# Performance work log

Measured on AMD Instinct MI355X. Metric: run time of the kernel, lower is better.

Reference implementation:

```python
import jax, jax.numpy as jnp
import numpy as np

HEAD_DIM = 256
N_HEADS = 8
ROPE_BASE = 10000.0
EPS = 1e-6


def _rms(x):
    xf = x.astype(jnp.float32)
    return xf * jax.lax.rsqrt(jnp.mean(xf * xf, axis=-1, keepdims=True) + EPS)


def _rotate_half(x):
    x1, x2 = jnp.split(x, 2, axis=-1)
    return jnp.concatenate([-x2, x1], axis=-1)


def _mlp(h, wg, wu, wd):
    # Gemma gated MLP with gelu_pytorch_tanh activation
    return (jax.nn.gelu(h @ wg, approximate=True) * (h @ wu)) @ wd


def _qkv(h, wq, wk, wv):
    B, S, _ = h.shape
    q = (h @ wq).reshape(B, S, N_HEADS, HEAD_DIM).transpose(0, 2, 1, 3)  # [B,H,S,Dh]
    k = (h @ wk).reshape(B, S, HEAD_DIM)                                  # MQA: 1 kv head
    v = (h @ wv).reshape(B, S, HEAD_DIM)
    return q, k, v


def _forward(x_prefix, x_expert, attention_mask, adarms_cond, position_ids,
             p_ln1, p_wq, p_wk, p_wv, p_wo, p_ln2, p_wgate, p_wup, p_wdown,
             e_ada1_w, e_ada1_b, e_wq, e_wk, e_wv, e_wo, e_ada2_w, e_ada2_b,
             e_wgate, e_wup, e_wdown):
    B, S1, Dp = x_prefix.shape
    S2 = x_expert.shape[1]

    # --- pre-attention norms: plain Gemma RMSNorm (prefix), AdaRMS (expert) ---
    h_p = _rms(x_prefix) * (1.0 + p_ln1)
    mod1 = adarms_cond @ e_ada1_w + e_ada1_b                  # [B, 3*De]
    sc1, sh1, g1 = jnp.split(mod1, 3, axis=-1)
    h_e = _rms(x_expert) * (1.0 + sc1[:, None]) + sh1[:, None]
    gate1_e = g1[:, None]                                      # [B,1,De]

    # --- concatenated QKV across the two streams ---
    q_p, k_p, v_p = _qkv(h_p, p_wq, p_wk, p_wv)
    q_e, k_e, v_e = _qkv(h_e, e_wq, e_wk, e_wv)
    q = jnp.concatenate([q_p, q_e], axis=2)                    # [B,H,S,Dh]
    k = jnp.concatenate([k_p, k_e], axis=1)                    # [B,S,Dh]
    v = jnp.concatenate([v_p, v_e], axis=1)

    # --- rotary embedding on joint positions ---
    inv_freq = 1.0 / (ROPE_BASE ** (jnp.arange(0, HEAD_DIM, 2, dtype=jnp.float32) / HEAD_DIM))
    ang = position_ids.astype(jnp.float32)[..., None] * inv_freq
    emb = jnp.concatenate([ang, ang], axis=-1)                 # [B,S,Dh]
    cos, sin = jnp.cos(emb), jnp.sin(emb)
    q = q * cos[:, None] + _rotate_half(q) * sin[:, None]
    k = k * cos + _rotate_half(k) * sin

    # --- eager MQA attention ---
    scaling = HEAD_DIM ** -0.5
    scores = jnp.einsum('bhqd,bkd->bhqk', q, k) * scaling + attention_mask
    probs = jax.nn.softmax(scores.astype(jnp.float32), axis=-1)
    att = jnp.einsum('bhqk,bkd->bhqd', probs, v)
    att = att.transpose(0, 2, 1, 3).reshape(B, S1 + S2, N_HEADS * HEAD_DIM)

    # --- prefix stream: o_proj, residual, RMSNorm, gated MLP, residual ---
    res_p = x_prefix + att[:, :S1] @ p_wo
    h2_p = _rms(res_p) * (1.0 + p_ln2)
    out_p = res_p + _mlp(h2_p, p_wgate, p_wup, p_wdown)

    # --- expert stream: gated residuals from AdaRMS ---
    res_e = x_expert + gate1_e * (att[:, S1:] @ e_wo)
    mod2 = adarms_cond @ e_ada2_w + e_ada2_b
    sc2, sh2, g2 = jnp.split(mod2, 3, axis=-1)
    h2_e = _rms(res_e) * (1.0 + sc2[:, None]) + sh2[:, None]
    out_e = res_e + g2[:, None] * _mlp(h2_e, e_wgate, e_wup, e_wdown)
    return out_p, out_e


def setup_inputs() -> dict:
    key = jax.random.key(0)
    ks = iter(jax.random.split(key, 32))
    B, S1, S2 = 4, 768, 64
    Dp, De, Dh, H = 2048, 1024, 256, 8
    Fp, Fe = 16384, 4096

    def w(shape, s=0.02):
        return jax.random.normal(next(ks), shape, dtype=jnp.float32) * s

    return dict(
        x_prefix=jax.random.normal(next(ks), (B, S1, Dp), dtype=jnp.float32),
        x_expert=jax.random.normal(next(ks), (B, S2, De), dtype=jnp.float32),
        attention_mask=jnp.zeros((B, 1, S1 + S2, S1 + S2), dtype=jnp.float32),
        adarms_cond=jax.random.normal(next(ks), (B, De), dtype=jnp.float32),
        position_ids=jnp.sort(jax.random.randint(next(ks), (B, S1 + S2), 0, S1 + S2), axis=-1),
        p_ln1=jnp.zeros((Dp,), jnp.float32),
        p_wq=w((Dp, H * Dh)), p_wk=w((Dp, Dh)), p_wv=w((Dp, Dh)), p_wo=w((H * Dh, Dp)),
        p_ln2=jnp.zeros((Dp,), jnp.float32),
        p_wgate=w((Dp, Fp)), p_wup=w((Dp, Fp)), p_wdown=w((Fp, Dp)),
        e_ada1_w=w((De, 3 * De)), e_ada1_b=jnp.zeros((3 * De,), jnp.float32),
        e_wq=w((De, H * Dh)), e_wk=w((De, Dh)), e_wv=w((De, Dh)), e_wo=w((H * Dh, De)),
        e_ada2_w=w((De, 3 * De)), e_ada2_b=jnp.zeros((3 * De,), jnp.float32),
        e_wgate=w((De, Fe)), e_wup=w((De, Fe)), e_wdown=w((Fe, De)),
    )


def reference(x_prefix, x_expert, attention_mask, adarms_cond, position_ids,
              p_ln1, p_wq, p_wk, p_wv, p_wo, p_ln2, p_wgate, p_wup, p_wdown,
              e_ada1_w, e_ada1_b, e_wq, e_wk, e_wv, e_wo, e_ada2_w, e_ada2_b,
              e_wgate, e_wup, e_wdown):
    return _forward(x_prefix, x_expert, attention_mask, adarms_cond, position_ids,
                    p_ln1, p_wq, p_wk, p_wv, p_wo, p_ln2, p_wgate, p_wup, p_wdown,
                    e_ada1_w, e_ada1_b, e_wq, e_wk, e_wv, e_wo, e_ada2_w, e_ada2_b,
                    e_wgate, e_wup, e_wdown)
```

## Files before the change

kernel.cpp:

```cpp
#include <hip/hip_runtime.h>
#include <stdint.h>

typedef unsigned short ushort_t;
typedef __attribute__((ext_vector_type(8))) short short8;
typedef __attribute__((ext_vector_type(4))) float f32x4;

#define DEVINL __device__ __forceinline__

DEVINL ushort_t f2bf(float f){
  union { float f; uint32_t u; } v; v.f = f;
  uint32_t u = v.u;
  uint32_t r = (u + 0x7fffu + ((u >> 16) & 1u)) >> 16;
  return (ushort_t)r;
}
DEVINL float bf2f(ushort_t h){
  union { uint32_t u; float f; } v; v.u = ((uint32_t)h) << 16;
  return v.f;
}
DEVINL f32x4 mfma16(short8 a, short8 b, f32x4 c){
  return __builtin_amdgcn_mfma_f32_16x16x32_bf16(a, b, c, 0, 0, 0);
}
DEVINL void gload_lds16(const void* g, void* l){
  __builtin_amdgcn_global_load_lds((const __attribute__((address_space(1))) void*)g,
                                   (__attribute__((address_space(3))) void*)l, 16, 0, 0);
}
DEVINL float gelu_tanh(float x){
  return 0.5f * x * (1.f + tanhf(0.7978845608028654f * (x + 0.044715f * x * x * x)));
}

#define BAR() __builtin_amdgcn_s_barrier()
#define LGK0() asm volatile("s_waitcnt lgkmcnt(0)" ::: "memory")
#define VMC4() asm volatile("s_waitcnt vmcnt(4)" ::: "memory")
#define VMC0() asm volatile("s_waitcnt vmcnt(0)" ::: "memory")
#define PRIO1() __builtin_amdgcn_s_setprio(1)
#define PRIO0() __builtin_amdgcn_s_setprio(0)

__global__ void transpose_bf16(const float* __restrict__ W, ushort_t* __restrict__ Wt,
                               int K, int N)
{
  __shared__ ushort_t tile[64 * 65];
  const int t = threadIdx.x;
  const int k0 = blockIdx.y * 64, n0 = blockIdx.x * 64;
#pragma unroll
  for (int rr = 0; rr < 4; ++rr){
    const int row = rr * 16 + (t >> 4);
    const int c4 = (t & 15) * 4;
    float4 v = *(const float4*)&W[(size_t)(k0 + row) * N + n0 + c4];
    ushort_t* dst = &tile[row * 65 + c4];
    dst[0] = f2bf(v.x); dst[1] = f2bf(v.y); dst[2] = f2bf(v.z); dst[3] = f2bf(v.w);
  }
  __syncthreads();
  const int n = t >> 2, kc = (t & 3) * 16;
  __align__(16) ushort_t tmp[16];
#pragma unroll
  for (int j = 0; j < 16; ++j) tmp[j] = tile[(kc + j) * 65 + n];
  ushort_t* out = &Wt[(size_t)(n0 + n) * K + k0 + kc];
  *(short8*)&out[0] = *(short8*)&tmp[0];
  *(short8*)&out[8] = *(short8*)&tmp[8];
}

__global__ void mod_kernel(const float* __restrict__ cond,
                           const float* __restrict__ w1, const float* __restrict__ b1,
                           const float* __restrict__ w2, const float* __restrict__ b2,
                           float* __restrict__ mod1, float* __restrict__ mod2)
{
  __shared__ float cs[1024];
  const int bid = blockIdx.x, tid = threadIdx.x;
  const int which = bid / 48, rem = bid % 48, b = rem / 12, j0 = (rem % 12) * 256;
  const float* W = which ? w2 : w1;
  const float* bias = which ? b2 : b1;
  float* out = which ? mod2 : mod1;
#pragma unroll
  for (int i = 0; i < 4; ++i) cs[i * 256 + tid] = cond[b * 1024 + i * 256 + tid];
  __syncthreads();
  const int j = j0 + tid;
  float acc = bias[j];
  for (int k = 0; k < 1024; ++k) acc = fmaf(cs[k], W[(size_t)k * 3072 + j], acc);
  out[b * 3072 + j] = acc;
}

__global__ void rms_kernel(const float* __restrict__ x, ushort_t* __restrict__ out, int D,
                           const float* __restrict__ sw, const float* __restrict__ sh,
                           int mod_rpb, int mod_stride)
{
  const int row = blockIdx.x, tid = threadIdx.x;
  const float* xr = x + (size_t)row * D;
  const int nc = D >> 10;
  float ss = 0.f;
  for (int c = 0; c < nc; ++c){
    float4 v = *(const float4*)&xr[c * 1024 + tid * 4];
    ss += v.x * v.x + v.y * v.y + v.z * v.z + v.w * v.w;
  }
  for (int o = 32; o > 0; o >>= 1) ss += __shfl_xor(ss, o);
  __shared__ float red[4];
  if ((tid & 63) == 0) red[tid >> 6] = ss;
  __syncthreads();
  const float scale = rsqrtf((red[0] + red[1] + red[2] + red[3]) / (float)D + 1e-6f);
  const float* swp = sw;
  const float* shp = sh;
  if (mod_rpb){
    int bb = row / mod_rpb;
    swp += (size_t)bb * mod_stride;
    if (shp) shp += (size_t)bb * mod_stride;
  }
  for (int c = 0; c < nc; ++c){
    const int d = c * 1024 + tid * 4;
    float4 v = *(const float4*)&xr[d];
    float vv[4] = {v.x, v.y, v.z, v.w};
#pragma unroll
    for (int i = 0; i < 4; ++i){
      float tv = vv[i] * scale * (1.f + swp[d + i]);
      if (shp) tv += shp[d + i];
      out[(size_t)row * D + d + i] = f2bf(tv);
    }
  }
}

__global__ void rope_kernel(const ushort_t* __restrict__ qkv_p, const ushort_t* __restrict__ qkv_e,
                            const int* __restrict__ pos_ids,
                            ushort_t* __restrict__ q_all, ushort_t* __restrict__ k_all,
                            ushort_t* __restrict__ vT)
{
  const int tok = blockIdx.x, tid = threadIdx.x;
  int b, s;
  const ushort_t* src;
  if (tok < 3072){ b = tok / 768; s = tok - b * 768; src = qkv_p + (size_t)tok * 2560; }
  else { int te = tok - 3072; b = te >> 6; s = 768 + (te & 63); src = qkv_e + (size_t)te * 2560; }
  const int pos = pos_ids[b * 832 + s];
  __shared__ float cs[128], sn[128];
  if (tid < 128){
    float f = powf(10000.f, -(float)tid * (1.f / 128.f));
    float a = (float)pos * f;
    cs[tid] = cosf(a); sn[tid] = sinf(a);
  }
  __syncthreads();
#pragma unroll
  for (int c = 0; c < 10; ++c){
    const int n = c * 256 + tid;
    const float v = bf2f(src[n]);
    if (n < 2048){
      const int h = n >> 8, d = n & 255;
      const float o = bf2f(src[(h << 8) + ((d < 128) ? (d + 128) : (d - 128))]);
      const int dd = d & 127;
      const float r = (d < 128) ? v * cs[dd] - o * sn[dd] : v * cs[dd] + o * sn[dd];
      q_all[(((size_t)(b * 8 + h)) * 832 + s) * 256 + d] = f2bf(r);
    } else if (n < 2304){
      const int d = n - 2048;
      const float o = bf2f(src[2048 + ((d < 128) ? (d + 128) : (d - 128))]);
      const int dd = d & 127;
      const float r = (d < 128) ? v * cs[dd] - o * sn[dd] : v * cs[dd] + o * sn[dd];
      const int ck = d >> 3, e = d & 7;
      const int ck2 = ck ^ (s & 7);
      k_all[((size_t)(b * 832) + s) * 256 + (ck2 << 3) + e] = f2bf(r);
    } else {
      const int d = n - 2304;
      const int stile = s >> 6, sl = s & 63;
      const int cv = sl >> 3, e = sl & 7;
      const int cv2 = cv ^ (d & 7);
      vT[((size_t)(b * 256) + d) * 832 + (stile << 6) + (cv2 << 3) + e] = src[n];
    }
  }
}

__global__ void __launch_bounds__(256, 2)
attn_kernel(const ushort_t* __restrict__ q_all, const ushort_t* __restrict__ k_all,
            const ushort_t* __restrict__ vT, const float* __restrict__ mask,
            ushort_t* __restrict__ att)
{
  __shared__ __align__(16) ushort_t Ks[64 * 256];
  __shared__ __align__(16) ushort_t Vs[256 * 64];
  __shared__ __align__(16) ushort_t Ps[4][16 * 72];
  const int tid = threadIdx.x, lane = tid & 63, wid = tid >> 6;
  const int l15 = lane & 15, lg = lane >> 4;
  const int qt = blockIdx.x, h = blockIdx.y, b = blockIdx.z;
  const int q0 = qt * 64 + wid * 16;
  const int x7 = l15 & 7;

  short8 qf[8];
  {
    const ushort_t* qr = q_all + (((size_t)(b * 8 + h) * 832) + q0 + l15) * 256;
#pragma unroll
    for (int s = 0; s < 8; ++s) qf[s] = *(const short8*)&qr[s * 32 + lg * 8];
  }

  f32x4 accO[16] = {};
  float mrow[4] = {-3.0e38f, -3.0e38f, -3.0e38f, -3.0e38f};
  float lrow[4] = {0.f, 0.f, 0.f, 0.f};

  for (int kt = 0; kt < 13; ++kt){
    const int s0 = kt * 64;
#pragma unroll
    for (int i = 0; i < 8; ++i){
      const int o = i * 256 + tid;
      gload_lds16(k_all + ((size_t)(b * 832) + s0 + (o >> 5)) * 256 + (o & 31) * 8, &Ks[o * 8]);
      gload_lds16(vT + ((size_t)(b * 256) + (o >> 3)) * 832 + s0 + (o & 7) * 8, &Vs[o * 8]);
    }
    __syncthreads();

    f32x4 sc[4] = {};
#pragma unroll
    for (int s = 0; s < 8; ++s){
#pragma unroll
      for (int nf = 0; nf < 4; ++nf){
        short8 kb = *(const short8*)&Ks[(nf * 16 + l15) * 256 + (((s * 4 + lg) ^ x7) << 3)];
        sc[nf] = mfma16(qf[s], kb, sc[nf]);
      }
    }
#pragma unroll
    for (int nf = 0; nf < 4; ++nf){
#pragma unroll
      for (int r = 0; r < 4; ++r){
        const int q = q0 + lg * 4 + r;
        const int kk = s0 + nf * 16 + l15;
        sc[nf][r] = sc[nf][r] * 0.0625f + mask[((size_t)b * 832 + q) * 832 + kk];
      }
    }
    float al[4];
#pragma unroll
    for (int r = 0; r < 4; ++r){
      float tm = fmaxf(fmaxf(sc[0][r], sc[1][r]), fmaxf(sc[2][r], sc[3][r]));
      tm = fmaxf(tm, __shfl_xor(tm, 1));
      tm = fmaxf(tm, __shfl_xor(tm, 2));
      tm = fmaxf(tm, __shfl_xor(tm, 4));
      tm = fmaxf(tm, __shfl_xor(tm, 8));
      const float mnew = fmaxf(mrow[r], tm);
      al[r] = __expf(mrow[r] - mnew);
      mrow[r] = mnew;
      float rs = 0.f;
#pragma unroll
      for (int nf = 0; nf < 4; ++nf){
        const float p = __expf(sc[nf][r] - mnew);
        rs += p;
        Ps[wid][(lg * 4 + r) * 72 + nf * 16 + l15] = f2bf(p);
      }
      rs += __shfl_xor(rs, 1);
      rs += __shfl_xor(rs, 2);
      rs += __shfl_xor(rs, 4);
      rs += __shfl_xor(rs, 8);
      lrow[r] = lrow[r] * al[r] + rs;
    }
#pragma unroll
    for (int nd = 0; nd < 16; ++nd){
#pragma unroll
      for (int r = 0; r < 4; ++r) accO[nd][r] *= al[r];
    }
#pragma unroll
    for (int ks = 0; ks < 2; ++ks){
      short8 pa = *(const short8*)&Ps[wid][l15 * 72 + ks * 32 + lg * 8];
#pragma unroll
      for (int nd = 0; nd < 16; ++nd){
        short8 vb = *(const short8*)&Vs[(nd * 16 + l15) * 64 + (((ks * 4 + lg) ^ x7) << 3)];
        accO[nd] = mfma16(pa, vb, accO[nd]);
      }
    }
    __syncthreads();
  }
#pragma unroll
  for (int nd = 0; nd < 16; ++nd){
#pragma unroll
    for (int r = 0; r < 4; ++r){
      const int q = q0 + lg * 4 + r;
      const int d = nd * 16 + l15;
      att[((size_t)(b * 832) + q) * 2048 + h * 256 + d] = f2bf(accO[nd][r] / lrow[r]);
    }
  }
}

template<int EPI>
__global__ void __launch_bounds__(256, 2)
gemm_bt(const ushort_t* __restrict__ A, int lda, int a_rpb, int a_bstride, int a_r0,
        const ushort_t* __restrict__ Bt, int ldb,
        void* __restrict__ Cv, int N, int K,
        const void* __restrict__ Xv,
        const float* __restrict__ gatep, int gate_stride, int gate_rpb,
        size_t pstride)
{
  __shared__ __align__(16) ushort_t As[128 * 64];
  __shared__ __align__(16) ushort_t Bs[128 * 64];
  const int tid = threadIdx.x;
  const int lane = tid & 63;
  const int l15 = lane & 15, lg = lane >> 4;
  const int wid = tid >> 6;
  const int wm = (wid >> 1) * 64, wn = (wid & 1) * 64;
  const int gx = gridDim.x, gy = gridDim.y, nwg = gx * gy;
  const int orig = blockIdx.y * gx + blockIdx.x;
  const int q = nwg >> 3, r = nwg & 7;
  const int xcd = orig & 7, lo = orig >> 3;
  const int wg = (xcd < r ? xcd * (q + 1) : r * (q + 1) + (xcd - r) * q) + lo;
  const int m0 = (wg % gy) * 128, n0 = (wg / gy) * 128;
  const int z = blockIdx.z;
  const int kbeg = z * K, kend = z * K + K;

  size_t abase[4], bbase[4];
  const int k8 = (tid & 7) * 8;
#pragma unroll
  for (int i = 0; i < 4; ++i){
    const int row = (i * 256 + tid) >> 3;
    const int rr = m0 + row;
    const int bb = rr / a_rpb;
    const int arow = bb * a_bstride + a_r0 + (rr - bb * a_rpb);
    abase[i] = (size_t)arow * lda + k8;
    bbase[i] = (size_t)(n0 + row) * ldb + k8;
  }

  f32x4 acc[4][4] = {};

  for (int kt = kbeg; kt < kend; kt += 64){
#pragma unroll
    for (int i = 0; i < 4; ++i){
      gload_lds16(A + abase[i] + kt, &As[(i * 256 + tid) * 8]);
      gload_lds16(Bt + bbase[i] + kt, &Bs[(i * 256 + tid) * 8]);
    }
    __syncthreads();
#pragma unroll
    for (int s = 0; s < 2; ++s){
      const int ko = s * 32 + lg * 8;
      short8 af[4], bfr[4];
#pragma unroll
      for (int i = 0; i < 4; ++i) af[i] = *(const short8*)&As[(wm + i * 16 + l15) * 64 + ko];
#pragma unroll
      for (int j = 0; j < 4; ++j) bfr[j] = *(const short8*)&Bs[(wn + j * 16 + l15) * 64 + ko];
#pragma unroll
      for (int i = 0; i < 4; ++i)
#pragma unroll
        for (int j = 0; j < 4; ++j)
          acc[i][j] = mfma16(af[i], bfr[j], acc[i][j]);
    }
    __syncthreads();
  }

#pragma unroll
  for (int i = 0; i < 4; ++i){
#pragma unroll
    for (int rr = 0; rr < 4; ++rr){
      const int m = m0 + wm + i * 16 + lg * 4 + rr;
#pragma unroll
      for (int j = 0; j < 4; ++j){
        const int n = n0 + wn + j * 16 + l15;
        const size_t idx = (size_t)m * N + n;
        const float v = acc[i][j][rr];
        if (EPI == 0){
          ((ushort_t*)Cv)[idx] = f2bf(v);
        } else if (EPI == 1){
          const float g = bf2f(((const ushort_t*)Xv)[idx]);
          ((ushort_t*)Cv)[idx] = f2bf(gelu_tanh(g) * v);
        } else if (EPI == 2){
          ((float*)Cv)[idx] = ((const float*)Xv)[idx] + v;
        } else if (EPI == 3){
          const int bb = m / gate_rpb;
          ((float*)Cv)[idx] = ((const float*)Xv)[idx] + gatep[(size_t)bb * gate_stride + n] * v;
        } else {
          ((float*)Cv)[(size_t)z * pstride + idx] = v;
        }
      }
    }
  }
}

#define MMAQ(AF, BF, MQ, NQ) \
  { _Pragma("unroll") for (int i_ = 0; i_ < 4; ++i_){ \
      _Pragma("unroll") for (int j_ = 0; j_ < 2; ++j_){ \
        _Pragma("unroll") for (int s_ = 0; s_ < 2; ++s_){ \
          acc[(MQ)*4 + i_][(NQ)*2 + j_] = \
            mfma16(AF[i_][s_], BF[j_][s_], acc[(MQ)*4 + i_][(NQ)*2 + j_]); } } } }

#define READA(F, BUF, OA) \
  { _Pragma("unroll") for (int i_ = 0; i_ < 4; ++i_){ \
      _Pragma("unroll") for (int s_ = 0; s_ < 2; ++s_){ \
        F[i_][s_] = *(const short8*)&(BUF)[OA[i_][s_]]; } } }

#define READB(F, BUF, OB) \
  { _Pragma("unroll") for (int j_ = 0; j_ < 2; ++j_){ \
      _Pragma("unroll") for (int s_ = 0; s_ < 2; ++s_){ \
        F[j_][s_] = *(const short8*)&(BUF)[OB[j_][s_]]; } } }

template<int EPI>
__global__ void __launch_bounds__(512, 1)
gemm8(const ushort_t* __restrict__ A, int lda,
      const ushort_t* __restrict__ Bt, int ldb,
      void* __restrict__ Cv, int N, int klen,
      const void* __restrict__ Xv, size_t pstride)
{
  __shared__ __align__(16) ushort_t As[2][256 * 64];
  __shared__ __align__(16) ushort_t Bs[2][256 * 64];

  const int tid = threadIdx.x;
  const int lane = tid & 63, wid = tid >> 6;
  const int l15 = lane & 15, lg = lane >> 4;
  const int wm = (wid >> 2) * 128, wn = (wid & 3) * 64;

  const int gx = gridDim.x, gy = gridDim.y, nwg = gx * gy;
  const int orig = blockIdx.y * gx + blockIdx.x;
  const int q = nwg >> 3, r = nwg & 7;
  const int xcd = orig & 7, lo = orig >> 3;
  const int wg = (xcd < r ? xcd * (q + 1) : r * (q + 1) + (xcd - r) * q) + lo;
  const int m0 = (wg % gy) * 256, n0 = (wg / gy) * 256;
  const int z = blockIdx.z;
  const size_t k0 = (size_t)z * klen;
  const int NT = klen >> 6;

  uint32_t offA0[4][2], offA1[4][2], offB0[2][2], offB1[2][2];
#pragma unroll
  for (int i = 0; i < 4; ++i){
#pragma unroll
    for (int s = 0; s < 2; ++s){
      int r0 = wm + 0 * 64 + i * 16 + l15;
      int r1 = wm + 1 * 64 + i * 16 + l15;
      offA0[i][s] = r0 * 64 + (((s * 4 + lg) ^ (r0 & 7)) << 3);
      offA1[i][s] = r1 * 64 + (((s * 4 + lg) ^ (r1 & 7)) << 3);
    }
  }
#pragma unroll
  for (int j = 0; j < 2; ++j){
#pragma unroll
    for (int s = 0; s < 2; ++s){
      int r0 = wn + 0 * 32 + j * 16 + l15;
      int r1 = wn + 1 * 32 + j * 16 + l15;
      offB0[j][s] = r0 * 64 + (((s * 4 + lg) ^ (r0 & 7)) << 3);
      offB1[j][s] = r1 * 64 + (((s * 4 + lg) ^ (r1 & 7)) << 3);
    }
  }

  const ushort_t* gptr[4][2];
  uint32_t ldso[2];
#pragma unroll
  for (int c = 0; c < 2; ++c){
    const int idx = c * 512 + tid;
    const int row = idx >> 3, slot = idx & 7;
    const uint32_t sw = (uint32_t)((slot ^ (row & 7)) << 3);
    ldso[c] = (uint32_t)idx * 8;
    gptr[0][c] = A  + (size_t)(m0 + row) * lda + k0 + sw;
    gptr[1][c] = A  + (size_t)(m0 + 128 + row) * lda + k0 + sw;
    gptr[2][c] = Bt + (size_t)(n0 + row) * ldb + k0 + sw;
    gptr[3][c] = Bt + (size_t)(n0 + 128 + row) * ldb + k0 + sw;
  }

  auto stage = [&](int buf, int half, int kt){
    ushort_t* base = (half < 2) ? &As[buf][(half & 1) * 8192] : &Bs[buf][(half & 1) * 8192];
#pragma unroll
    for (int c = 0; c < 2; ++c)
      gload_lds16(gptr[half][c] + kt, base + ldso[c]);
  };

  stage(0, 0, 0); stage(0, 1, 0); stage(0, 2, 0); stage(0, 3, 0);
  if (NT > 1){ stage(1, 2, 64); stage(1, 3, 64); VMC4(); } else { VMC0(); }
  BAR();

  short8 af[4][2], bq0[2][2], bq1[2][2];
  f32x4 acc[8][4] = {};

  for (int t = 0; t < NT; ++t){
    const int cur = t & 1, nxt = cur ^ 1;
    const int kc1 = (t + 1) << 6, kc2 = (t + 2) << 6;
    const ushort_t* Ac = As[cur];
    const ushort_t* Bc = Bs[cur];
    READA(af, Ac, offA0);
    READB(bq0, Bc, offB0);
    READB(bq1, Bc, offB1);
    if (t + 1 < NT){ stage(nxt, 0, kc1); stage(nxt, 1, kc1); }
    BAR(); LGK0();
    PRIO1(); MMAQ(af, bq0, 0, 0); MMAQ(af, bq1, 0, 1); PRIO0(); BAR();
    READA(af, Ac, offA1);
    if (t + 2 < NT){ stage(cur, 2, kc2); stage(cur, 3, kc2); VMC4(); } else { VMC0(); }
    BAR(); LGK0();
    PRIO1(); MMAQ(af, bq1, 1, 1); MMAQ(af, bq0, 1, 0); PRIO0(); BAR();
  }

#pragma unroll
  for (int i = 0; i < 8; ++i){
#pragma unroll
    for (int rr = 0; rr < 4; ++rr){
      const int m = m0 + wm + i * 16 + lg * 4 + rr;
#pragma unroll
      for (int j = 0; j < 4; ++j){
        const int n = n0 + wn + j * 16 + l15;
        const size_t idx = (size_t)m * N + n;
        const float v = acc[i][j][rr];
        if (EPI == 0){
          ((ushort_t*)Cv)[idx] = f2bf(v);
        } else if (EPI == 1){
          const float g = bf2f(((const ushort_t*)Xv)[idx]);
          ((ushort_t*)Cv)[idx] = f2bf(gelu_tanh(g) * v);
        } else {
          ((float*)Cv)[(size_t)z * pstride + idx] = v;
        }
      }
    }
  }
}

__global__ void reduce4(const float* __restrict__ part, const float* __restrict__ res,
                        float* __restrict__ out, int total4, size_t pstride)
{
  int i = blockIdx.x * blockDim.x + threadIdx.x;
  const int stride = gridDim.x * blockDim.x;
  for (; i < total4; i += stride){
    const size_t e = (size_t)i * 4;
    float4 a = *(const float4*)&res[e];
#pragma unroll
    for (int z = 0; z < 4; ++z){
      float4 p = *(const float4*)&part[(size_t)z * pstride + e];
      a.x += p.x; a.y += p.y; a.z += p.z; a.w += p.w;
    }
    *(float4*)&out[e] = a;
  }
}

__global__ void fuse_gelu(const float* __restrict__ pg, const float* __restrict__ pu,
                          ushort_t* __restrict__ out, int total4, size_t pstride)
{
  int i = blockIdx.x * blockDim.x + threadIdx.x;
  const int stride = gridDim.x * blockDim.x;
  for (; i < total4; i += stride){
    const size_t e = (size_t)i * 4;
    float4 g = *(const float4*)&pg[e];
    float4 u = *(const float4*)&pu[e];
#pragma unroll
    for (int z = 1; z < 4; ++z){
      float4 a = *(const float4*)&pg[(size_t)z * pstride + e];
      float4 b = *(const float4*)&pu[(size_t)z * pstride + e];
      g.x += a.x; g.y += a.y; g.z += a.z; g.w += a.w;
      u.x += b.x; u.y += b.y; u.z += b.z; u.w += b.w;
    }
    out[e + 0] = f2bf(gelu_tanh(g.x) * u.x);
    out[e + 1] = f2bf(gelu_tanh(g.y) * u.y);
    out[e + 2] = f2bf(gelu_tanh(g.z) * u.z);
    out[e + 3] = f2bf(gelu_tanh(g.w) * u.w);
  }
}

__global__ void reduce_gated(const float* __restrict__ part, size_t pstride, int nz,
                             const float* __restrict__ base, const float* __restrict__ gate,
                             int gstride, int rpb, int N,
                             float* __restrict__ out, int total4)
{
  int i = blockIdx.x * blockDim.x + threadIdx.x;
  const int stride = gridDim.x * blockDim.x;
  for (; i < total4; i += stride){
    const size_t e = (size_t)i * 4;
    const int row = (int)(e / N), n = (int)(e % N);
    const int b = row / rpb;
    float4 s = *(const float4*)&part[e];
    for (int z = 1; z < nz; ++z){
      float4 p = *(const float4*)&part[(size_t)z * pstride + e];
      s.x += p.x; s.y += p.y; s.z += p.z; s.w += p.w;
    }
    float4 bs = *(const float4*)&base[e];
    const float* gp = &gate[(size_t)b * gstride + n];
    bs.x += gp[0] * s.x; bs.y += gp[1] * s.y; bs.z += gp[2] * s.z; bs.w += gp[3] * s.w;
    *(float4*)&out[e] = bs;
  }
}

extern "C" void kernel_launch(void* const* d_in, const int* in_sizes, int n_in,
                              void* d_out, int out_size, void* d_ws, size_t ws_size,
                              hipStream_t stream)
{
  const float* x_prefix = (const float*)d_in[0];
  const float* x_expert = (const float*)d_in[1];
  const float* mask     = (const float*)d_in[2];
  const float* cond     = (const float*)d_in[3];
  const int*   pos      = (const int*)d_in[4];
  const float* p_ln1    = (const float*)d_in[5];
  const float* p_wq     = (const float*)d_in[6];
  const float* p_wk     = (const float*)d_in[7];
  const float* p_wv     = (const float*)d_in[8];
  const float* p_wo     = (const float*)d_in[9];
  const float* p_ln2    = (const float*)d_in[10];
  const float* p_wgate  = (const float*)d_in[11];
  const float* p_wup    = (const float*)d_in[12];
  const float* p_wdown  = (const float*)d_in[13];
  const float* e_ada1_w = (const float*)d_in[14];
  const float* e_ada1_b = (const float*)d_in[15];
  const float* e_wq     = (const float*)d_in[16];
  const float* e_wk     = (const float*)d_in[17];
  const float* e_wv     = (const float*)d_in[18];
  const float* e_wo     = (const float*)d_in[19];
  const float* e_ada2_w = (const float*)d_in[20];
  const float* e_ada2_b = (const float*)d_in[21];
  const float* e_wgate  = (const float*)d_in[22];
  const float* e_wup    = (const float*)d_in[23];
  const float* e_wdown  = (const float*)d_in[24];

  char* ws = (char*)d_ws;
  size_t off = 0;
  auto alloc = [&](size_t bytes) -> char* {
    char* p = ws + off;
    off += bytes;
    off = (off + 255) & ~(size_t)255;
    return p;
  };

  ushort_t* t_wqkv_p  = (ushort_t*)alloc((size_t)2560 * 2048 * 2);
  ushort_t* t_wo_p    = (ushort_t*)alloc((size_t)2048 * 2048 * 2);
  ushort_t* t_wgate_p = (ushort_t*)alloc((size_t)16384 * 2048 * 2);
  ushort_t* t_wup_p   = (ushort_t*)alloc((size_t)16384 * 2048 * 2);
  ushort_t* t_wdown_p = (ushort_t*)alloc((size_t)2048 * 16384 * 2);
  ushort_t* t_wqkv_e  = (ushort_t*)alloc((size_t)2560 * 1024 * 2);
  ushort_t* t_wo_e    = (ushort_t*)alloc((size_t)1024 * 2048 * 2);
  ushort_t* t_wgate_e = (ushort_t*)alloc((size_t)4096 * 1024 * 2);
  ushort_t* t_wup_e   = (ushort_t*)alloc((size_t)4096 * 1024 * 2);
  ushort_t* t_wdown_e = (ushort_t*)alloc((size_t)1024 * 4096 * 2);
  float* mod1 = (float*)alloc((size_t)4 * 3072 * 4);
  float* mod2 = (float*)alloc((size_t)4 * 3072 * 4);
  float* res_p = (float*)alloc((size_t)3072 * 2048 * 4);
  float* res_e = (float*)alloc((size_t)256 * 1024 * 4);
  ushort_t* h2_p = (ushort_t*)alloc((size_t)3072 * 2048 * 2);
  ushort_t* h2_e = (ushort_t*)alloc((size_t)256 * 1024 * 2);
  ushort_t* g_e  = (ushort_t*)alloc((size_t)256 * 4096 * 2);

  const size_t zone_off = off;
  ushort_t* h_p   = (ushort_t*)alloc((size_t)3072 * 2048 * 2);
  ushort_t* h_e   = (ushort_t*)alloc((size_t)256 * 1024 * 2);
  ushort_t* qkv_p = (ushort_t*)alloc((size_t)3072 * 2560 * 2);
  ushort_t* qkv_e = (ushort_t*)alloc((size_t)256 * 2560 * 2);
  ushort_t* q_all = (ushort_t*)alloc((size_t)4 * 8 * 832 * 256 * 2);
  ushort_t* k_all = (ushort_t*)alloc((size_t)4 * 832 * 256 * 2);
  ushort_t* vTb   = (ushort_t*)alloc((size_t)4 * 256 * 832 * 2);
  ushort_t* att   = (ushort_t*)alloc((size_t)4 * 832 * 2048 * 2);
  const size_t phase1_end = off;
  ushort_t* g_p = (ushort_t*)(ws + zone_off);

  float* partials = (float*)t_wgate_p;
  const size_t PSTRIDE_P = (size_t)3072 * 2048;
  float* pwo = (float*)(ws + zone_off);
  const size_t PSTRIDE_E = (size_t)256 * 1024;
  float* pg = (float*)t_wgate_p;
  float* pu = pg + (size_t)4 * 256 * 4096;
  float* pd = pu + (size_t)4 * 256 * 4096;
  const size_t PSTRIDE_GE = (size_t)256 * 4096;

  const size_t g_p_end = zone_off + (size_t)3072 * 16384 * 2;
  const size_t needed = (phase1_end > g_p_end) ? phase1_end : g_p_end;
  if (ws_size < needed) return;

  const int BIG = 1 << 30;

  transpose_bf16<<<dim3(2048/64, 2048/64), 256, 0, stream>>>(p_wq, t_wqkv_p, 2048, 2048);
  transpose_bf16<<<dim3(256/64, 2048/64), 256, 0, stream>>>(p_wk, t_wqkv_p + (size_t)2048*2048, 2048, 256);
  transpose_bf16<<<dim3(256/64, 2048/64), 256, 0, stream>>>(p_wv, t_wqkv_p + (size_t)2304*2048, 2048, 256);
  transpose_bf16<<<dim3(2048/64, 2048/64), 256, 0, stream>>>(p_wo, t_wo_p, 2048, 2048);
  transpose_bf16<<<dim3(16384/64, 2048/64), 256, 0, stream>>>(p_wgate, t_wgate_p, 2048, 16384);
  transpose_bf16<<<dim3(16384/64, 2048/64), 256, 0, stream>>>(p_wup, t_wup_p, 2048, 16384);
  transpose_bf16<<<dim3(2048/64, 16384/64), 256, 0, stream>>>(p_wdown, t_wdown_p, 16384, 2048);
  transpose_bf16<<<dim3(2048/64, 1024/64), 256, 0, stream>>>(e_wq, t_wqkv_e, 1024, 2048);
  transpose_bf16<<<dim3(256/64, 1024/64), 256, 0, stream>>>(e_wk, t_wqkv_e + (size_t)2048*1024, 1024, 256);
  transpose_bf16<<<dim3(256/64, 1024/64), 256, 0, stream>>>(e_wv, t_wqkv_e + (size_t)2304*1024, 1024, 256);
  transpose_bf16<<<dim3(1024/64, 2048/64), 256, 0, stream>>>(e_wo, t_wo_e, 2048, 1024);
  transpose_bf16<<<dim3(4096/64, 1024/64), 256, 0, stream>>>(e_wgate, t_wgate_e, 1024, 4096);
  transpose_bf16<<<dim3(4096/64, 1024/64), 256, 0, stream>>>(e_wup, t_wup_e, 1024, 4096);
  transpose_bf16<<<dim3(1024/64, 4096/64), 256, 0, stream>>>(e_wdown, t_wdown_e, 4096, 1024);

  mod_kernel<<<96, 256, 0, stream>>>(cond, e_ada1_w, e_ada1_b, e_ada2_w, e_ada2_b, mod1, mod2);

  rms_kernel<<<3072, 256, 0, stream>>>(x_prefix, h_p, 2048, p_ln1, nullptr, 0, 0);
  rms_kernel<<<256, 256, 0, stream>>>(x_expert, h_e, 1024, mod1, mod1 + 1024, 64, 3072);

  gemm_bt<0><<<dim3(20, 24), 256, 0, stream>>>(h_p, 2048, BIG, 0, 0, t_wqkv_p, 2048,
                                               qkv_p, 2560, 2048, nullptr, nullptr, 0, 1, 0);
  gemm_bt<0><<<dim3(20, 2), 256, 0, stream>>>(h_e, 1024, BIG, 0, 0, t_wqkv_e, 1024,
                                              qkv_e, 2560, 1024, nullptr, nullptr, 0, 1, 0);

  rope_kernel<<<3328, 256, 0, stream>>>(qkv_p, qkv_e, pos, q_all, k_all, vTb);

  attn_kernel<<<dim3(13, 8, 4), 256, 0, stream>>>(q_all, k_all, vTb, mask, att);

  gemm_bt<2><<<dim3(16, 24), 256, 0, stream>>>(att, 2048, 768, 832, 0, t_wo_p, 2048,
                                               res_p, 2048, 2048, x_prefix, nullptr, 0, 1, 0);
  gemm_bt<4><<<dim3(8, 2, 4), 256, 0, stream>>>(att, 2048, 64, 832, 768, t_wo_e, 2048,
                                                pwo, 1024, 512, nullptr, nullptr, 0, 1, PSTRIDE_E);
  reduce_gated<<<256, 256, 0, stream>>>(pwo, PSTRIDE_E, 4, x_expert, mod1 + 2048, 3072, 64, 1024,
                                        res_e, (256 * 1024) / 4);

  rms_kernel<<<3072, 256, 0, stream>>>(res_p, h2_p, 2048, p_ln2, nullptr, 0, 0);
  rms_kernel<<<256, 256, 0, stream>>>(res_e, h2_e, 1024, mod2, mod2 + 1024, 64, 3072);

  gemm8<0><<<dim3(64, 12, 1), 512, 0, stream>>>(h2_p, 2048, t_wgate_p, 2048,
                                                g_p, 16384, 2048, nullptr, 0);
  gemm8<1><<<dim3(64, 12, 1), 512, 0, stream>>>(h2_p, 2048, t_wup_p, 2048,
                                                g_p, 16384, 2048, g_p, 0);
  gemm8<4><<<dim3(8, 12, 4), 512, 0, stream>>>(g_p, 16384, t_wdown_p, 16384,
                                               partials, 2048, 4096, nullptr, PSTRIDE_P);
  reduce4<<<2048, 256, 0, stream>>>(partials, res_p, (float*)d_out,
                                    (3072 * 2048) / 4, PSTRIDE_P);

  gemm_bt<4><<<dim3(32, 2, 4), 256, 0, stream>>>(h2_e, 1024, BIG, 0, 0, t_wgate_e, 1024,
                                                 pg, 4096, 256, nullptr, nullptr, 0, 1, PSTRIDE_GE);
  gemm_bt<4><<<dim3(32, 2, 4), 256, 0, stream>>>(h2_e, 1024, BIG, 0, 0, t_wup_e, 1024,
                                                 pu, 4096, 256, nullptr, nullptr, 0, 1, PSTRIDE_GE);
  fuse_gelu<<<1024, 256, 0, stream>>>(pg, pu, g_e, (256 * 4096) / 4, PSTRIDE_GE);
  gemm_bt<4><<<dim3(8, 2, 8), 256, 0, stream>>>(g_e, 4096, BIG, 0, 0, t_wdown_e, 4096,
                                                pd, 1024, 512, nullptr, nullptr, 0, 1, PSTRIDE_E);
  reduce_gated<<<256, 256, 0, stream>>>(pd, PSTRIDE_E, 8, res_e, mod2 + 2048, 3072, 64, 1024,
                                        (float*)d_out + (size_t)3072 * 2048, (256 * 1024) / 4);
}
```

Before: 1.269 ms.

## Fuse prefix down-proj residual into GEMM, merge expert gate/up GEMMs

The prefix down projection moves from a split-K gemm8 with a separate reduce4 pass to a single gemm_bt<2> launch that adds the residual in its epilogue and writes straight to the output. The expert gate and up projections become one launch, which assumes t_wup_e sits right after t_wgate_e so the combined N is 8192. fuse_gelu now reads an interleaved gate/up partial buffer. This removes fp32 partial traffic and a launch, but swaps the tuned 512-thread gemm8 for gemm_bt on the largest GEMM with K=16384 and no split-K.

```diff
diff --git a/kernel.cpp b/kernel.cpp
--- a/kernel.cpp
+++ b/kernel.cpp
@@ -489,36 +489,22 @@
   }
 }
 
-__global__ void reduce4(const float* __restrict__ part, const float* __restrict__ res,
-                        float* __restrict__ out, int total4, size_t pstride)
+__global__ void fuse_gelu(const float* __restrict__ P, ushort_t* __restrict__ out,
+                          int total4, size_t zstride)
 {
   int i = blockIdx.x * blockDim.x + threadIdx.x;
   const int stride = gridDim.x * blockDim.x;
   for (; i < total4; i += stride){
     const size_t e = (size_t)i * 4;
-    float4 a = *(const float4*)&res[e];
-#pragma unroll
-    for (int z = 0; z < 4; ++z){
-      float4 p = *(const float4*)&part[(size_t)z * pstride + e];
-      a.x += p.x; a.y += p.y; a.z += p.z; a.w += p.w;
-    }
-    *(float4*)&out[e] = a;
-  }
-}
-
-__global__ void fuse_gelu(const float* __restrict__ pg, const float* __restrict__ pu,
-                          ushort_t* __restrict__ out, int total4, size_t pstride)
-{
-  int i = blockIdx.x * blockDim.x + threadIdx.x;
-  const int stride = gridDim.x * blockDim.x;
-  for (; i < total4; i += stride){
-    const size_t e = (size_t)i * 4;
-    float4 g = *(const float4*)&pg[e];
-    float4 u = *(const float4*)&pu[e];
+    const int row = (int)(e >> 12);
+    const int n   = (int)(e & 4095);
+    const size_t gb = (size_t)row * 8192 + n;
+    float4 g = *(const float4*)&P[gb];
+    float4 u = *(const float4*)&P[gb + 4096];
 #pragma unroll
     for (int z = 1; z < 4; ++z){
-      float4 a = *(const float4*)&pg[(size_t)z * pstride + e];
-      float4 b = *(const float4*)&pu[(size_t)z * pstride + e];
+      float4 a = *(const float4*)&P[(size_t)z * zstride + gb];
+      float4 b = *(const float4*)&P[(size_t)z * zstride + gb + 4096];
       g.x += a.x; g.y += a.y; g.z += a.z; g.w += a.w;
       u.x += b.x; u.y += b.y; u.z += b.z; u.w += b.w;
     }
@@ -621,14 +607,11 @@
   const size_t phase1_end = off;
   ushort_t* g_p = (ushort_t*)(ws + zone_off);
 
-  float* partials = (float*)t_wgate_p;
-  const size_t PSTRIDE_P = (size_t)3072 * 2048;
   float* pwo = (float*)(ws + zone_off);
   const size_t PSTRIDE_E = (size_t)256 * 1024;
-  float* pg = (float*)t_wgate_p;
-  float* pu = pg + (size_t)4 * 256 * 4096;
-  float* pd = pu + (size_t)4 * 256 * 4096;
-  const size_t PSTRIDE_GE = (size_t)256 * 4096;
+  float* pgu = (float*)t_wgate_p;
+  const size_t PSTRIDE_GU = (size_t)256 * 8192;
+  float* pd = pgu + (size_t)4 * PSTRIDE_GU;
 
   const size_t g_p_end = zone_off + (size_t)3072 * 16384 * 2;
   const size_t needed = (phase1_end > g_p_end) ? phase1_end : g_p_end;
@@ -679,16 +662,12 @@
                                                 g_p, 16384, 2048, nullptr, 0);
   gemm8<1><<<dim3(64, 12, 1), 512, 0, stream>>>(h2_p, 2048, t_wup_p, 2048,
                                                 g_p, 16384, 2048, g_p, 0);
-  gemm8<4><<<dim3(8, 12, 4), 512, 0, stream>>>(g_p, 16384, t_wdown_p, 16384,
-                                               partials, 2048, 4096, nullptr, PSTRIDE_P);
-  reduce4<<<2048, 256, 0, stream>>>(partials, res_p, (float*)d_out,
-                                    (3072 * 2048) / 4, PSTRIDE_P);
-
-  gemm_bt<4><<<dim3(32, 2, 4), 256, 0, stream>>>(h2_e, 1024, BIG, 0, 0, t_wgate_e, 1024,
-                                                 pg, 4096, 256, nullptr, nullptr, 0, 1, PSTRIDE_GE);
-  gemm_bt<4><<<dim3(32, 2, 4), 256, 0, stream>>>(h2_e, 1024, BIG, 0, 0, t_wup_e, 1024,
-                                                 pu, 4096, 256, nullptr, nullptr, 0, 1, PSTRIDE_GE);
-  fuse_gelu<<<1024, 256, 0, stream>>>(pg, pu, g_e, (256 * 4096) / 4, PSTRIDE_GE);
+  gemm_bt<2><<<dim3(16, 24), 256, 0, stream>>>(g_p, 16384, BIG, 0, 0, t_wdown_p, 16384,
+                                               (float*)d_out, 2048, 16384, res_p, nullptr, 0, 1, 0);
+
+  gemm_bt<4><<<dim3(64, 2, 4), 256, 0, stream>>>(h2_e, 1024, BIG, 0, 0, t_wgate_e, 1024,
+                                                 pgu, 8192, 256, nullptr, nullptr, 0, 1, PSTRIDE_GU);
+  fuse_gelu<<<1024, 256, 0, stream>>>(pgu, g_e, (256 * 4096) / 4, PSTRIDE_GU);
   gemm_bt<4><<<dim3(8, 2, 8), 256, 0, stream>>>(g_e, 4096, BIG, 0, 0, t_wdown_e, 4096,
                                                 pd, 1024, 512, nullptr, nullptr, 0, 1, PSTRIDE_E);
   reduce_gated<<<256, 256, 0, stream>>>(pd, PSTRIDE_E, 8, res_e, mod2 + 2048, 3072, 64, 1024,
```

Result: slower. 1.449 ms (+14.2%).
